# Performance work log

Hardware: AMD Instinct MI355X
Metric: run time of the kernel (lower is better)

The kernel has to match this reference:

```python
import jax, jax.numpy as jnp
import numpy as np

EPS = 1e-5
TEMPERATURE = 1.0

def _finger_masks():
    # (5, 21) anatomical hyperedge masks: fingers cover node indices 1..20 in groups of 4
    m = np.zeros((5, 21), np.float32)
    for i in range(5):
        m[i, 1 + 4 * i: 5 + 4 * i] = 1.0
    return jnp.asarray(m)

def setup_inputs() -> dict:
    key = jax.random.key(0)
    ks = jax.random.split(key, 13)
    N, C, T, V, E = 128, 128, 256, 21, 8
    return {
        "x": jax.random.normal(ks[0], (N, C, T, V), jnp.float32),
        "dyn_w": jax.random.normal(ks[1], (E, C), jnp.float32) * 0.05,
        "dyn_b": jax.random.normal(ks[2], (E,), jnp.float32) * 0.05,
        "dyn_gamma": jax.random.uniform(ks[3], (E,), jnp.float32, 0.5, 1.5),
        "dyn_beta": jax.random.normal(ks[4], (E,), jnp.float32) * 0.05,
        "dyn_mean": jax.random.normal(ks[5], (E,), jnp.float32) * 0.05,
        "dyn_var": jax.random.uniform(ks[6], (E,), jnp.float32, 0.5, 1.5),
        "ft_w": jax.random.normal(ks[7], (C, C), jnp.float32) * 0.05,
        "ft_b": jax.random.normal(ks[8], (C,), jnp.float32) * 0.05,
        "ft_gamma": jax.random.uniform(ks[9], (C,), jnp.float32, 0.5, 1.5),
        "ft_beta": jax.random.normal(ks[10], (C,), jnp.float32) * 0.05,
        "ft_mean": jax.random.normal(ks[11], (C,), jnp.float32) * 0.05,
        "ft_var": jax.random.uniform(ks[12], (C,), jnp.float32, 0.5, 1.5),
    }

def reference(x, dyn_w, dyn_b, dyn_gamma, dyn_beta, dyn_mean, dyn_var,
              ft_w, ft_b, ft_gamma, ft_beta, ft_mean, ft_var):
    N = x.shape[0]
    # dynamic hyperedge generation: mean over T -> conv1x1 -> BN -> ReLU -> softmax over V
    xm = x.mean(axis=2)                                         # (N, C, V)
    h = jnp.einsum('ncv,ec->nev', xm, dyn_w) + dyn_b[None, :, None]
    scale = dyn_gamma * jax.lax.rsqrt(dyn_var + EPS)
    h = (h - dyn_mean[None, :, None]) * scale[None, :, None] + dyn_beta[None, :, None]
    h = jax.nn.relu(h)
    H_dyn = jax.nn.softmax(h / TEMPERATURE, axis=-1)            # (N, E, V)
    H_phy = jnp.broadcast_to(_finger_masks()[None], (N, 5, 21))
    H = jnp.concatenate([H_dyn, H_phy], axis=1)                 # (N, M=E+5, V)
    # feature transform: conv1x1 -> BN -> ReLU
    xf = jnp.einsum('nctv,oc->notv', x, ft_w) + ft_b[None, :, None, None]
    fscale = ft_gamma * jax.lax.rsqrt(ft_var + EPS)
    xf = (xf - ft_mean[None, :, None, None]) * fscale[None, :, None, None] + ft_beta[None, :, None, None]
    xf = jax.nn.relu(xf)                                        # (N, Cout, T, V)
    # hypergraph message passing: node -> edge -> node
    Y = jnp.einsum('nmv,nctv->ncmt', H, xf)                     # (N, Cout, M, T)
    Xr = jnp.einsum('nmv,ncmt->nctv', H, Y)                     # (N, Cout, T, V)
    return Xr + x  # residual (in_channels == out_channels)
```

## Files before the change

### kernel.cpp

```cpp
#include <hip/hip_runtime.h>
#include <hip/hip_bf16.h>
#include <math.h>

#define EPS 1e-5f

static constexpr int N_ = 128, C_ = 128, T_ = 256, V_ = 21, E_ = 8, M_ = 13;
static constexpr int TV_ = T_ * V_;
static constexpr int NT_ = 8;
static constexpr int ST_ = NT_ * V_;
static constexpr int SP_ = 176;
static constexpr int XF_PITCH_F = 178;

typedef short bf16x8 __attribute__((ext_vector_type(8)));
typedef short s16x4  __attribute__((ext_vector_type(4)));
typedef float f32x4  __attribute__((ext_vector_type(4)));

__device__ inline short f2bf(float v) {
    __hip_bfloat16 b = __float2bfloat16(v);
    return *reinterpret_cast<short*>(&b);
}

__global__ __launch_bounds__(256) void prep_kernel(
    const float* __restrict__ ft_w, const float* __restrict__ ft_b,
    const float* __restrict__ ft_gamma, const float* __restrict__ ft_beta,
    const float* __restrict__ ft_mean, const float* __restrict__ ft_var,
    __hip_bfloat16* __restrict__ w_bf, float* __restrict__ sc_g, float* __restrict__ sh_g)
{
    int tid = blockIdx.x * 256 + threadIdx.x;
    if (tid < C_ * C_) w_bf[tid] = __float2bfloat16(ft_w[tid]);
    if (tid < C_) {
        float sc = ft_gamma[tid] * rsqrtf(ft_var[tid] + EPS);
        sc_g[tid] = sc;
        sh_g[tid] = (ft_b[tid] - ft_mean[tid]) * sc + ft_beta[tid];
    }
}

__global__ __launch_bounds__(256) void mean_kernel(const float* __restrict__ x,
                                                   float* __restrict__ xm) {
    __shared__ float slab[TV_];
    __shared__ float partial[V_ * 8];
    const int nc = blockIdx.x;
    const int tid = threadIdx.x;
    const float4* src4 = (const float4*)(x + (size_t)nc * TV_);
    float4* slab4 = (float4*)slab;
    #pragma unroll
    for (int it = 0; it < 6; ++it) {
        int idx = it * 256 + tid;
        if (idx < TV_ / 4) slab4[idx] = src4[idx];
    }
    __syncthreads();
    if (tid < V_ * 8) {
        int v = tid >> 3, g = tid & 7;
        float s = 0.f;
        #pragma unroll
        for (int tt = 0; tt < 32; ++tt) s += slab[(g * 32 + tt) * V_ + v];
        partial[v * 8 + g] = s;
    }
    __syncthreads();
    if (tid < V_) {
        float s = 0.f;
        #pragma unroll
        for (int g = 0; g < 8; ++g) s += partial[tid * 8 + g];
        xm[(size_t)nc * V_ + tid] = s * (1.0f / T_);
    }
}

__global__ __launch_bounds__(64) void hyper_kernel(
    const float* __restrict__ xm, const float* __restrict__ dyn_w,
    const float* __restrict__ dyn_b,
    const float* __restrict__ dyn_gamma, const float* __restrict__ dyn_beta,
    const float* __restrict__ dyn_mean, const float* __restrict__ dyn_var,
    float* __restrict__ A_out)
{
    __shared__ float xs[C_ * V_];
    __shared__ float Hs[M_ * V_];
    const int n = blockIdx.x;
    const int l = threadIdx.x;
    const float* src = xm + (size_t)n * C_ * V_;
    for (int idx = l; idx < C_ * V_; idx += 64) xs[idx] = src[idx];
    __syncthreads();
    for (int idx = l; idx < E_ * V_; idx += 64) {
        int e = idx / V_, v = idx - e * V_;
        float acc = 0.f;
        for (int c = 0; c < C_; ++c) acc = fmaf(xs[c * V_ + v], dyn_w[e * C_ + c], acc);
        acc += dyn_b[e];
        float scale = dyn_gamma[e] * rsqrtf(dyn_var[e] + EPS);
        acc = (acc - dyn_mean[e]) * scale + dyn_beta[e];
        Hs[idx] = fmaxf(acc, 0.f);
    }
    __syncthreads();
    if (l < E_) {
        float row[V_];
        float mx = -1e30f;
        #pragma unroll
        for (int v = 0; v < V_; ++v) { row[v] = Hs[l * V_ + v]; mx = fmaxf(mx, row[v]); }
        float s = 0.f;
        #pragma unroll
        for (int v = 0; v < V_; ++v) { row[v] = __expf(row[v] - mx); s += row[v]; }
        float inv = 1.0f / s;
        #pragma unroll
        for (int v = 0; v < V_; ++v) Hs[l * V_ + v] = row[v] * inv;
    } else if (l < M_) {
        int i = l - E_;
        #pragma unroll
        for (int v = 0; v < V_; ++v)
            Hs[l * V_ + v] = (v >= 1 + 4 * i && v < 5 + 4 * i) ? 1.0f : 0.0f;
    }
    __syncthreads();
    for (int idx = l; idx < V_ * V_; idx += 64) {
        int u = idx / V_, w = idx - u * V_;
        float s = 0.f;
        #pragma unroll
        for (int m = 0; m < M_; ++m) s = fmaf(Hs[m * V_ + u], Hs[m * V_ + w], s);
        A_out[(size_t)n * V_ * V_ + idx] = s;
    }
}

__global__ __launch_bounds__(512) void main_kernel(
    const float* __restrict__ x, const __hip_bfloat16* __restrict__ w_bf,
    const float* __restrict__ sc_g, const float* __restrict__ sh_g,
    const float* __restrict__ A_g, float* __restrict__ out)
{
    __shared__ __align__(16) char lds[64 * XF_PITCH_F * 4];
    __shared__ float A_s[V_ * V_];
    __shared__ float sc_s[C_], sh_s[C_];

    const int st = blockIdx.x;
    const int n  = blockIdx.y;
    const int tid = threadIdx.x;
    const int w = tid >> 6;
    const int l = tid & 63;
    const int s0 = st * ST_;
    const size_t xbase = (size_t)n * C_ * TV_ + s0;

    if (tid < C_) { sc_s[tid] = sc_g[tid]; sh_s[tid] = sh_g[tid]; }
    for (int i = tid; i < V_ * V_; i += 512) A_s[i] = A_g[(size_t)n * V_ * V_ + i];

    const int o_row = 16 * w + (l & 15);
    const int hi = l >> 4;
    const int coff0 = 8 * hi;
    bf16x8 wf[4];
    #pragma unroll
    for (int kk = 0; kk < 4; ++kk)
        wf[kk] = *(const bf16x8*)((const short*)w_bf + o_row * C_ + kk * 32 + coff0);

    for (int idx = tid; idx < (C_ / 4) * (ST_ / 4); idx += 512) {
        int cg = idx / (ST_ / 4), q = idx - cg * (ST_ / 4);
        int c0 = cg * 4, sq = q * 4;
        f32x4 f[4];
        #pragma unroll
        for (int i = 0; i < 4; ++i)
            f[i] = *(const f32x4*)(x + xbase + (size_t)(c0 + i) * TV_ + sq);
        #pragma unroll
        for (int i = 0; i < 4; ++i) {
            int s = sq + i;
            s16x4 pk;
            #pragma unroll
            for (int j = 0; j < 4; ++j) pk[j] = f2bf(f[j][i]);
            int byte = (s * 256 + c0 * 2) ^ ((s & 7) << 4);
            *(s16x4*)(lds + byte) = pk;
        }
    }
    if (tid < 256) {
        int s = ST_ + (tid >> 5);
        int c4 = (tid & 31) * 4;
        int byte = (s * 256 + c4 * 2) ^ ((s & 7) << 4);
        *(unsigned long long*)(lds + byte) = 0ull;
    }
    __syncthreads();

    f32x4 acc[11];
    #pragma unroll
    for (int nf = 0; nf < 11; ++nf) acc[nf] = (f32x4){0.f, 0.f, 0.f, 0.f};
    #pragma unroll
    for (int kk = 0; kk < 4; ++kk) {
        #pragma unroll
        for (int nf = 0; nf < 11; ++nf) {
            int srow = 16 * nf + (l & 15);
            int byte = (srow * 256 + (kk * 32 + coff0) * 2) ^ ((srow & 7) << 4);
            bf16x8 b = *(const bf16x8*)(lds + byte);
            acc[nf] = __builtin_amdgcn_mfma_f32_16x16x32_bf16(wf[kk], b, acc[nf], 0, 0, 0);
        }
    }

    const int obase = 16 * w + 4 * hi;
    const int obase_local = obase & 63;
    float scr[4], shr[4];
    #pragma unroll
    for (int r = 0; r < 4; ++r) { scr[r] = sc_s[obase + r]; shr[r] = sh_s[obase + r]; }
    float* lds_f = (float*)lds;

    #pragma unroll
    for (int pass = 0; pass < 2; ++pass) {
        __syncthreads();
        if ((w >> 2) == pass) {
            #pragma unroll
            for (int nf = 0; nf < 11; ++nf) {
                int s = 16 * nf + (l & 15);
                if (s < ST_) {
                    #pragma unroll
                    for (int r = 0; r < 4; ++r) {
                        float vv = fmaxf(fmaf(acc[nf][r], scr[r], shr[r]), 0.f);
                        lds_f[(obase_local + r) * XF_PITCH_F + s] = vv;
                    }
                }
            }
        }
        __syncthreads();
        for (int idx = tid; idx < 64 * ST_; idx += 512) {
            int o2 = idx / ST_, s = idx - o2 * ST_;
            int t = s / V_, v = s - t * V_;
            const float* xrow = lds_f + o2 * XF_PITCH_F + t * V_;
            float sum = 0.f;
            #pragma unroll
            for (int u = 0; u < V_; ++u) sum = fmaf(xrow[u], A_s[u * V_ + v], sum);
            size_t g = xbase + (size_t)(pass * 64 + o2) * TV_ + s;
            out[g] = sum + x[g];
        }
    }
}

extern "C" void kernel_launch(void* const* d_in, const int* in_sizes, int n_in,
                              void* d_out, int out_size, void* d_ws, size_t ws_size,
                              hipStream_t stream) {
    const float* x         = (const float*)d_in[0];
    const float* dyn_w     = (const float*)d_in[1];
    const float* dyn_b     = (const float*)d_in[2];
    const float* dyn_gamma = (const float*)d_in[3];
    const float* dyn_beta  = (const float*)d_in[4];
    const float* dyn_mean  = (const float*)d_in[5];
    const float* dyn_var   = (const float*)d_in[6];
    const float* ft_w      = (const float*)d_in[7];
    const float* ft_b      = (const float*)d_in[8];
    const float* ft_gamma  = (const float*)d_in[9];
    const float* ft_beta   = (const float*)d_in[10];
    const float* ft_mean   = (const float*)d_in[11];
    const float* ft_var    = (const float*)d_in[12];
    float* out = (float*)d_out;

    char* ws = (char*)d_ws;
    float* xm  = (float*)ws;                                   ws += (size_t)N_ * C_ * V_ * 4;
    float* A_g = (float*)ws;                                   ws += (size_t)N_ * V_ * V_ * 4;
    __hip_bfloat16* w_bf = (__hip_bfloat16*)ws;                ws += (size_t)C_ * C_ * 2;
    float* sc_g = (float*)ws;                                  ws += C_ * 4;
    float* sh_g = (float*)ws;                                  ws += C_ * 4;

    prep_kernel<<<64, 256, 0, stream>>>(ft_w, ft_b, ft_gamma, ft_beta, ft_mean, ft_var,
                                        w_bf, sc_g, sh_g);
    mean_kernel<<<N_ * C_, 256, 0, stream>>>(x, xm);
    hyper_kernel<<<N_, 64, 0, stream>>>(xm, dyn_w, dyn_b, dyn_gamma, dyn_beta,
                                        dyn_mean, dyn_var, A_g);
    main_kernel<<<dim3(32, 128), 512, 0, stream>>>(x, w_bf, sc_g, sh_g, A_g, out);
}
```

Before: 416.9 us.

## Apply hypergraph adjacency via bf16 MFMA instead of scalar FMA loop

The second stage (multiplying the feature-transformed tile by the 21x21 node adjacency A = H^T H) moves from a scalar 21-term FMA loop over fp32 LDS to MFMA 16x16x32 bf16. The hyper kernel now emits A as a zero-padded 32x32 bf16 matrix, and the main kernel writes xf in bf16 with a padded row layout so all 128 channels are processed in one pass instead of two. This removes most scalar ALU and LDS traffic in the epilogue, at the cost of bf16 rounding of both xf and A, which adds numerical error.

```diff
diff --git a/kernel.cpp b/kernel.cpp
--- a/kernel.cpp
+++ b/kernel.cpp
@@ -8,8 +8,7 @@
 static constexpr int TV_ = T_ * V_;
 static constexpr int NT_ = 8;
 static constexpr int ST_ = NT_ * V_;
-static constexpr int SP_ = 176;
-static constexpr int XF_PITCH_F = 178;
+static constexpr int XF_PITCH = 48;
 
 typedef short bf16x8 __attribute__((ext_vector_type(8)));
 typedef short s16x4  __attribute__((ext_vector_type(4)));
@@ -70,7 +69,7 @@
     const float* __restrict__ dyn_b,
     const float* __restrict__ dyn_gamma, const float* __restrict__ dyn_beta,
     const float* __restrict__ dyn_mean, const float* __restrict__ dyn_var,
-    float* __restrict__ A_out)
+    __hip_bfloat16* __restrict__ A_bf)
 {
     __shared__ float xs[C_ * V_];
     __shared__ float Hs[M_ * V_];
@@ -107,22 +106,23 @@
             Hs[l * V_ + v] = (v >= 1 + 4 * i && v < 5 + 4 * i) ? 1.0f : 0.0f;
     }
     __syncthreads();
-    for (int idx = l; idx < V_ * V_; idx += 64) {
-        int u = idx / V_, w = idx - u * V_;
-        float s = 0.f;
-        #pragma unroll
-        for (int m = 0; m < M_; ++m) s = fmaf(Hs[m * V_ + u], Hs[m * V_ + w], s);
-        A_out[(size_t)n * V_ * V_ + idx] = s;
+    for (int idx = l; idx < 32 * 32; idx += 64) {
+        int u = idx >> 5, v = idx & 31;
+        float s = 0.f;
+        if (u < V_ && v < V_) {
+            #pragma unroll
+            for (int m = 0; m < M_; ++m) s = fmaf(Hs[m * V_ + u], Hs[m * V_ + v], s);
+        }
+        A_bf[(size_t)n * 1024 + idx] = __float2bfloat16(s);
     }
 }
 
 __global__ __launch_bounds__(512) void main_kernel(
     const float* __restrict__ x, const __hip_bfloat16* __restrict__ w_bf,
     const float* __restrict__ sc_g, const float* __restrict__ sh_g,
-    const float* __restrict__ A_g, float* __restrict__ out)
+    const __hip_bfloat16* __restrict__ A_bf, float* __restrict__ out)
 {
-    __shared__ __align__(16) char lds[64 * XF_PITCH_F * 4];
-    __shared__ float A_s[V_ * V_];
+    __shared__ __align__(16) char lds[49280];
     __shared__ float sc_s[C_], sh_s[C_];
 
     const int st = blockIdx.x;
@@ -130,19 +130,22 @@
     const int tid = threadIdx.x;
     const int w = tid >> 6;
     const int l = tid & 63;
+    const int hi = l >> 4;
+    const int lo = l & 15;
     const int s0 = st * ST_;
     const size_t xbase = (size_t)n * C_ * TV_ + s0;
 
     if (tid < C_) { sc_s[tid] = sc_g[tid]; sh_s[tid] = sh_g[tid]; }
-    for (int i = tid; i < V_ * V_; i += 512) A_s[i] = A_g[(size_t)n * V_ * V_ + i];
-
-    const int o_row = 16 * w + (l & 15);
-    const int hi = l >> 4;
-    const int coff0 = 8 * hi;
+
+    const int o_row = 16 * w + lo;
     bf16x8 wf[4];
     #pragma unroll
     for (int kk = 0; kk < 4; ++kk)
-        wf[kk] = *(const bf16x8*)((const short*)w_bf + o_row * C_ + kk * 32 + coff0);
+        wf[kk] = *(const bf16x8*)((const short*)w_bf + o_row * C_ + kk * 32 + 8 * hi);
+
+    const short* Abf_n = (const short*)A_bf + (size_t)n * 1024;
+    const bf16x8 bA0 = *(const bf16x8*)(Abf_n + lo * 32 + 8 * hi);
+    const bf16x8 bA1 = *(const bf16x8*)(Abf_n + (16 + lo) * 32 + 8 * hi);
 
     for (int idx = tid; idx < (C_ / 4) * (ST_ / 4); idx += 512) {
         int cg = idx / (ST_ / 4), q = idx - cg * (ST_ / 4);
@@ -176,46 +179,57 @@
     for (int kk = 0; kk < 4; ++kk) {
         #pragma unroll
         for (int nf = 0; nf < 11; ++nf) {
-            int srow = 16 * nf + (l & 15);
-            int byte = (srow * 256 + (kk * 32 + coff0) * 2) ^ ((srow & 7) << 4);
+            int srow = 16 * nf + lo;
+            int byte = (srow * 256 + (kk * 32 + 8 * hi) * 2) ^ ((srow & 7) << 4);
             bf16x8 b = *(const bf16x8*)(lds + byte);
             acc[nf] = __builtin_amdgcn_mfma_f32_16x16x32_bf16(wf[kk], b, acc[nf], 0, 0, 0);
         }
     }
+    __syncthreads();
 
     const int obase = 16 * w + 4 * hi;
-    const int obase_local = obase & 63;
     float scr[4], shr[4];
     #pragma unroll
     for (int r = 0; r < 4; ++r) { scr[r] = sc_s[obase + r]; shr[r] = sh_s[obase + r]; }
-    float* lds_f = (float*)lds;
-
-    #pragma unroll
-    for (int pass = 0; pass < 2; ++pass) {
-        __syncthreads();
-        if ((w >> 2) == pass) {
+    #pragma unroll
+    for (int nf = 0; nf < 11; ++nf) {
+        int s = 16 * nf + lo;
+        if (s < ST_) {
+            int t = s / V_, u = s - t * V_;
             #pragma unroll
-            for (int nf = 0; nf < 11; ++nf) {
-                int s = 16 * nf + (l & 15);
-                if (s < ST_) {
-                    #pragma unroll
-                    for (int r = 0; r < 4; ++r) {
-                        float vv = fmaxf(fmaf(acc[nf][r], scr[r], shr[r]), 0.f);
-                        lds_f[(obase_local + r) * XF_PITCH_F + s] = vv;
-                    }
-                }
+            for (int r = 0; r < 4; ++r) {
+                float vv = fmaxf(fmaf(acc[nf][r], scr[r], shr[r]), 0.f);
+                *(short*)(lds + ((obase + r) * 8 + t) * XF_PITCH + u * 2) = f2bf(vv);
             }
         }
-        __syncthreads();
-        for (int idx = tid; idx < 64 * ST_; idx += 512) {
-            int o2 = idx / ST_, s = idx - o2 * ST_;
-            int t = s / V_, v = s - t * V_;
-            const float* xrow = lds_f + o2 * XF_PITCH_F + t * V_;
-            float sum = 0.f;
-            #pragma unroll
-            for (int u = 0; u < V_; ++u) sum = fmaf(xrow[u], A_s[u * V_ + v], sum);
-            size_t g = xbase + (size_t)(pass * 64 + o2) * TV_ + s;
-            out[g] = sum + x[g];
+    }
+    for (int row = tid; row < 1024; row += 512) {
+        *(short*)(lds + row * XF_PITCH + 42) = 0;
+        *(int*)(lds + row * XF_PITCH + 44) = 0;
+    }
+    if (tid < 4) *(int*)(lds + 49152 + tid * 4) = 0;
+    __syncthreads();
+
+    bf16x8 xfr[8];
+    #pragma unroll
+    for (int i = 0; i < 8; ++i) {
+        int row = 16 * (8 * w + i) + lo;
+        xfr[i] = *(const bf16x8*)(lds + row * XF_PITCH + 16 * hi);
+    }
+    #pragma unroll
+    for (int i = 0; i < 8; ++i) {
+        f32x4 d0 = (f32x4){0.f, 0.f, 0.f, 0.f};
+        f32x4 d1 = (f32x4){0.f, 0.f, 0.f, 0.f};
+        d0 = __builtin_amdgcn_mfma_f32_16x16x32_bf16(xfr[i], bA0, d0, 0, 0, 0);
+        d1 = __builtin_amdgcn_mfma_f32_16x16x32_bf16(xfr[i], bA1, d1, 0, 0, 0);
+        int row0 = 16 * (8 * w + i) + 4 * hi;
+        #pragma unroll
+        for (int r = 0; r < 4; ++r) {
+            int row = row0 + r;
+            int o = row >> 3, t = row & 7;
+            size_t g = xbase + (size_t)o * TV_ + t * V_;
+            out[g + lo] = d0[r] + x[g + lo];
+            if (lo < V_ - 16) out[g + 16 + lo] = d1[r] + x[g + 16 + lo];
         }
     }
 }
@@ -240,7 +254,7 @@
 
     char* ws = (char*)d_ws;
     float* xm  = (float*)ws;                                   ws += (size_t)N_ * C_ * V_ * 4;
-    float* A_g = (float*)ws;                                   ws += (size_t)N_ * V_ * V_ * 4;
+    __hip_bfloat16* A_bf = (__hip_bfloat16*)ws;                ws += (size_t)N_ * 1024 * 2;
     __hip_bfloat16* w_bf = (__hip_bfloat16*)ws;                ws += (size_t)C_ * C_ * 2;
     float* sc_g = (float*)ws;                                  ws += C_ * 4;
     float* sh_g = (float*)ws;                                  ws += C_ * 4;
@@ -249,6 +263,6 @@
                                         w_bf, sc_g, sh_g);
     mean_kernel<<<N_ * C_, 256, 0, stream>>>(x, xm);
     hyper_kernel<<<N_, 64, 0, stream>>>(xm, dyn_w, dyn_b, dyn_gamma, dyn_beta,
-                                        dyn_mean, dyn_var, A_g);
-    main_kernel<<<dim3(32, 128), 512, 0, stream>>>(x, w_bf, sc_g, sh_g, A_g, out);
-}
+                                        dyn_mean, dyn_var, A_bf);
+    main_kernel<<<dim3(32, 128), 512, 0, stream>>>(x, w_bf, sc_g, sh_g, A_bf, out);
+}
```

After: 336.8 us. -19.2%, faster.
